# Kernel tuning notes

Hardware: AMD Instinct MI355X
Metric: run time of the kernel (lower is better)

## Reference

```python
import jax, jax.numpy as jnp
import numpy as np

EMB = 1024
HID = 1536
NE = 8


def setup_inputs() -> dict:
    key = jax.random.key(0)
    ks = jax.random.split(key, 8)
    B, N, E, H, ne = 4, 2048, EMB, HID, NE
    s = 1.0 / np.sqrt(E)
    sh = 1.0 / np.sqrt(H)
    return {
        "x": jax.random.normal(ks[0], (B, N, E), dtype=jnp.float32),
        "Wr": jax.random.uniform(ks[1], (E, ne), minval=-s, maxval=s, dtype=jnp.float32),
        "br": jax.random.uniform(ks[2], (ne,), minval=-s, maxval=s, dtype=jnp.float32),
        "W1": jax.random.uniform(ks[3], (ne, E, H), minval=-s, maxval=s, dtype=jnp.float32),
        "b1": jax.random.uniform(ks[4], (ne, H), minval=-s, maxval=s, dtype=jnp.float32),
        "W2": jax.random.uniform(ks[5], (ne, H, E), minval=-sh, maxval=sh, dtype=jnp.float32),
        "b2": jax.random.uniform(ks[6], (ne, E), minval=-sh, maxval=sh, dtype=jnp.float32),
        "k": 2,
    }


def reference(x, Wr, br, W1, b1, W2, b2, k):
    B, N, E = x.shape
    T = B * N
    ne = Wr.shape[1]
    flat = x.reshape(T, E)
    logits = flat @ Wr + br                      # [T, ne]
    _, topk_idx = jax.lax.top_k(logits, k)       # [T, k]
    # counts[t, e] = number of top-k slots of token t assigned to expert e
    counts = jax.nn.one_hot(topk_idx, ne, dtype=flat.dtype).sum(axis=1)  # [T, ne]
    out = jnp.zeros_like(flat)
    for e in range(ne):  # small fixed loop over experts (structurally distinct weights)
        h = jax.nn.gelu(flat @ W1[e] + b1[e], approximate=False)  # torch nn.GELU = exact erf
        y = h @ W2[e] + b2[e]
        out = out + counts[:, e:e + 1] * y
    out = out / k
    return out.reshape(B, N, E)
```

## Files before the change

kernel.cpp:

```cpp
#include <hip/hip_runtime.h>
#include <hip/hip_bf16.h>
#include <math.h>

#define T_TOK 8192
#define EMB   1024
#define HID   1536
#define NE    8
#define NBINB 64
#define BINTOK (T_TOK / NBINB)

typedef float  floatx4 __attribute__((ext_vector_type(4)));
typedef __bf16 bf16x8  __attribute__((ext_vector_type(8)));

#define WS_COUNTS   0
#define WS_OFFSETS  1024
#define WS_FLAGS    2048
#define WS_BHIST    4096
#define WS_TOKMAP   8192
#define WS_TOKLIST  270336
#define WS_YBUF     532480
#define WS_W1T      34086912
#define WS_W2T      59252736
#define WS_H        84418560
#define WS_NEEDED   135143424

__device__ __forceinline__ float eload(const void* p, size_t idx, bool f32) {
  return f32 ? ((const float*)p)[idx] : (float)(((const __bf16*)p)[idx]);
}

__device__ __forceinline__ void glds16(const void* g, void* l) {
  __builtin_amdgcn_global_load_lds(
      (const __attribute__((address_space(1))) unsigned int*)g,
      (__attribute__((address_space(3))) unsigned int*)l, 16, 0, 0);
}

__global__ __launch_bounds__(256)
void sniff_kernel(const void* p0, const void* p1, const void* p2, const void* p3,
                  const void* p4, const void* p5, const void* p6, int* flags) {
  const void* ps[7] = {p0, p1, p2, p3, p4, p5, p6};
  const int nelem[7] = {T_TOK * EMB, EMB * NE, NE, NE * EMB * HID, NE * HID, NE * HID * EMB, NE * EMB};
  int t = blockIdx.x;
  const unsigned* w = (const unsigned*)ps[t];
  int nw = nelem[t] / 2;
  if (nw > 2048) nw = 2048;
  __shared__ int s_pl, s_nz;
  if (threadIdx.x == 0) { s_pl = 0; s_nz = 0; }
  __syncthreads();
  int pl = 0, nz = 0;
  for (int i = threadIdx.x; i < nw; i += 256) {
    unsigned v = w[i];
    if (v == 0) continue;
    nz++;
    unsigned e = (v >> 23) & 0xFF;
    if (e >= 100 && e <= 150) pl++;
  }
  atomicAdd(&s_pl, pl);
  atomicAdd(&s_nz, nz);
  __syncthreads();
  if (threadIdx.x == 0) flags[t] = (2 * s_pl > s_nz) ? 1 : 0;
}

__global__ __launch_bounds__(256)
void logits_kernel(const void* __restrict__ x, const void* __restrict__ Wr,
                   const void* __restrict__ br, const int* __restrict__ kptr,
                   const int* __restrict__ flags, int* __restrict__ topk,
                   __bf16* __restrict__ xbf) {
  const bool xf32  = flags[0] != 0;
  const bool wrf32 = flags[1] != 0;
  const bool brf32 = flags[2] != 0;
  const int wave = threadIdx.x >> 6;
  const int lane = threadIdx.x & 63;
  const int t = blockIdx.x * 4 + wave;

  float xv[16];
  {
    size_t base = (size_t)t * EMB + lane * 16;
    if (xf32) {
      const float* g = (const float*)x + base;
#pragma unroll
      for (int j = 0; j < 16; ++j) xv[j] = g[j];
    } else {
      bf16x8 u = *(const bf16x8*)((const __bf16*)x + base);
      bf16x8 v = *(const bf16x8*)((const __bf16*)x + base + 8);
#pragma unroll
      for (int j = 0; j < 8; ++j) { xv[j] = (float)u[j]; xv[8 + j] = (float)v[j]; }
    }
  }
  {
    bf16x8 o0, o1;
#pragma unroll
    for (int j = 0; j < 8; ++j) { o0[j] = (__bf16)xv[j]; o1[j] = (__bf16)xv[8 + j]; }
    __bf16* xo = xbf + (size_t)t * EMB + lane * 16;
    *(bf16x8*)xo = o0;
    *(bf16x8*)(xo + 8) = o1;
  }
  float acc[NE];
#pragma unroll
  for (int e = 0; e < NE; ++e) acc[e] = 0.f;
  if (wrf32) {
#pragma unroll
    for (int j = 0; j < 16; ++j) {
      const float* wr = (const float*)Wr + (size_t)(lane * 16 + j) * NE;
#pragma unroll
      for (int e = 0; e < NE; ++e) acc[e] += xv[j] * wr[e];
    }
  } else {
#pragma unroll
    for (int j = 0; j < 16; ++j) {
      bf16x8 wr = *(const bf16x8*)((const __bf16*)Wr + (size_t)(lane * 16 + j) * NE);
#pragma unroll
      for (int e = 0; e < NE; ++e) acc[e] += xv[j] * (float)wr[e];
    }
  }
#pragma unroll
  for (int e = 0; e < NE; ++e) {
#pragma unroll
    for (int off = 32; off > 0; off >>= 1)
      acc[e] += __shfl_xor(acc[e], off, 64);
  }
  if (lane == 0) {
    int k = kptr[0];
    if (k < 1) k = 1; if (k > NE) k = NE;
    float lg[NE];
#pragma unroll
    for (int e = 0; e < NE; ++e) lg[e] = acc[e] + eload(br, e, brf32);
    for (int s = 0; s < k; ++s) {
      int bi = 0; float bv = lg[0];
#pragma unroll
      for (int e = 1; e < NE; ++e) { if (lg[e] > bv) { bv = lg[e]; bi = e; } }
      lg[bi] = -3.0e38f;
      topk[t * 8 + s] = bi;
    }
  }
}

__global__ __launch_bounds__(128)
void bin1_kernel(const int* __restrict__ topk, const int* __restrict__ kptr,
                 int* __restrict__ bhist) {
  __shared__ int lhist[NE];
  if (threadIdx.x < NE) lhist[threadIdx.x] = 0;
  __syncthreads();
  int k = kptr[0];
  if (k < 1) k = 1; if (k > NE) k = NE;
  const int t = blockIdx.x * BINTOK + threadIdx.x;
  for (int s = 0; s < k; ++s) atomicAdd(&lhist[topk[t * 8 + s] & 7], 1);
  __syncthreads();
  if (threadIdx.x < NE) bhist[blockIdx.x * NE + threadIdx.x] = lhist[threadIdx.x];
}

__global__ __launch_bounds__(256)
void scan_kernel(int* __restrict__ bhist, int* __restrict__ counts, int* __restrict__ offsets) {
  __shared__ int sh[NBINB * NE];
  __shared__ int scnt[NE];
  __shared__ int soff[NE + 1];
  const int tid = threadIdx.x;
  for (int i = tid; i < NBINB * NE; i += 256) sh[i] = bhist[i];
  __syncthreads();
  if (tid < NE) {
    int s = 0;
    for (int b = 0; b < NBINB; ++b) s += sh[b * NE + tid];
    scnt[tid] = s;
  }
  __syncthreads();
  if (tid == 0) {
    int s = 0;
    for (int e = 0; e < NE; ++e) { soff[e] = s; s += scnt[e]; }
    soff[NE] = s;
  }
  __syncthreads();
  if (tid < NE) {
    int run = soff[tid];
    for (int b = 0; b < NBINB; ++b) {
      int v = sh[b * NE + tid];
      sh[b * NE + tid] = run;
      run += v;
    }
  }
  __syncthreads();
  for (int i = tid; i < NBINB * NE; i += 256) bhist[i] = sh[i];
  if (tid < NE) counts[tid] = scnt[tid];
  if (tid < NE + 1) offsets[tid] = soff[tid];
}

__global__ __launch_bounds__(128)
void bin2_kernel(const int* __restrict__ bhist, const int* __restrict__ offsets,
                 const int* __restrict__ kptr,
                 int* __restrict__ tok_list, int* __restrict__ tokmap) {
  __shared__ int lbase[NE];
  __shared__ int lcnt[NE];
  if (threadIdx.x < NE) {
    lbase[threadIdx.x] = bhist[blockIdx.x * NE + threadIdx.x];
    lcnt[threadIdx.x] = 0;
  }
  __syncthreads();
  int k = kptr[0];
  if (k < 1) k = 1; if (k > NE) k = NE;
  const int t = blockIdx.x * BINTOK + threadIdx.x;
  for (int s = 0; s < k; ++s) {
    int e = tokmap[t * 8 + s] & 7;
    int pos = atomicAdd(&lcnt[e], 1);
    int grow = lbase[e] + pos;
    tok_list[e * T_TOK + (grow - offsets[e])] = t;
    tokmap[t * 8 + s] = (e << 16) | grow;
  }
}

__global__ __launch_bounds__(256)
void transpose_kernel(const void* __restrict__ in, __bf16* __restrict__ out, int K, int N,
                      const int* __restrict__ flags, int fidx) {
  const bool f32 = flags[fidx] != 0;
  __shared__ __bf16 tile[64][65];
  size_t eoff = (size_t)blockIdx.z * (size_t)K * (size_t)N;
  int n0 = blockIdx.x * 64;
  int k0 = blockIdx.y * 64;
  int tx = threadIdx.x & 63;
  int ty = threadIdx.x >> 6;
#pragma unroll
  for (int i = 0; i < 16; ++i) {
    int r = i * 4 + ty;
    tile[r][tx] = (__bf16)eload(in, eoff + (size_t)(k0 + r) * N + (n0 + tx), f32);
  }
  __syncthreads();
#pragma unroll
  for (int i = 0; i < 16; ++i) {
    int r = i * 4 + ty;
    out[eoff + (size_t)(n0 + r) * K + (k0 + tx)] = tile[tx][r];
  }
}


#define STAGE4(TT) do {                                                  \
    const int _sl = (TT) & 3;                                            \
    __bf16* _dA = ldsA + _sl * 8192 + wave * 512;                        \
    __bf16* _dB = ldsB + _sl * 8192 + wave * 512;                        \
    const size_t _ko = (size_t)(TT) * 32;                                \
    glds16(pA0 + _ko, _dA);                                              \
    glds16(pA1 + _ko, _dA + 4096);                                       \
    glds16(pB0 + _ko, _dB);                                              \
    glds16(pB1 + _ko, _dB + 4096);                                       \
  } while (0)

#define KSTEP(TT, WAITS, DOSTAGE) do {                                   \
    asm volatile(WAITS ::: "memory");                                    \
    __builtin_amdgcn_s_barrier();                                        \
    const char* _aS = (const char*)(ldsA + ((TT) & 3) * 8192);           \
    const char* _bS = (const char*)(ldsB + ((TT) & 3) * 8192);           \
    bf16x8 _af[8], _bf[4];                                               \
    _Pragma("unroll")                                                    \
    for (int _i = 0; _i < 8; ++_i) _af[_i] = *(const bf16x8*)(_aS + aOff[_i]); \
    _Pragma("unroll")                                                    \
    for (int _j = 0; _j < 4; ++_j) _bf[_j] = *(const bf16x8*)(_bS + bOff[_j]); \
    if (DOSTAGE) STAGE4((TT) + 3);                                       \
    __builtin_amdgcn_s_setprio(1);                                       \
    _Pragma("unroll")                                                    \
    for (int _i = 0; _i < 8; ++_i)                                       \
      _Pragma("unroll")                                                  \
      for (int _j = 0; _j < 4; ++_j)                                     \
        acc[_i][_j] = __builtin_amdgcn_mfma_f32_16x16x32_bf16(_af[_i], _bf[_j], acc[_i][_j], 0, 0, 0); \
    __builtin_amdgcn_s_setprio(0);                                       \
  } while (0)

__global__ __launch_bounds__(512, 2)
void gemm1_kernel(const __bf16* __restrict__ xbf, const __bf16* __restrict__ w1t,
                  const void* __restrict__ b1, const int* __restrict__ counts,
                  const int* __restrict__ offsets, const int* __restrict__ tok_list,
                  const int* __restrict__ flags, __bf16* __restrict__ hbuf) {
  const int flat = blockIdx.x;
  const int e   = flat & 7;
  const int idx = flat >> 3;
  const int mT  = idx / 6;
  const int nT  = idx % 6;
  const int cnt = counts[e];
  if (mT * 256 >= cnt) return;
  const bool b1f32 = flags[4] != 0;

  __shared__ __align__(16) __bf16 ldsA[4 * 8192];
  __shared__ __align__(16) __bf16 ldsB[4 * 8192];

  const int tid  = threadIdx.x;
  const int wave = tid >> 6;
  const int lane = tid & 63;

  const int sr = wave * 16 + (lane >> 2);
  const int cA = lane & 3;
  const int cg = cA ^ ((sr >> 1) & 3);
  const int tokA0 = tok_list[e * T_TOK + mT * 256 + sr];
  const int tokA1 = tok_list[e * T_TOK + mT * 256 + 128 + sr];
  const __bf16* pA0 = xbf + (size_t)tokA0 * EMB + cg * 8;
  const __bf16* pA1 = xbf + (size_t)tokA1 * EMB + cg * 8;
  const __bf16* pB0 = w1t + ((size_t)e * HID + nT * 256 + sr) * EMB + cg * 8;
  const __bf16* pB1 = w1t + ((size_t)e * HID + nT * 256 + 128 + sr) * EMB + cg * 8;

  const int wm = (wave >> 2) * 128;
  const int wn = (wave & 3) * 64;
  const int fr = lane & 15;
  const int fc = lane >> 4;
  int aOff[8], bOff[4];
#pragma unroll
  for (int i = 0; i < 8; ++i) { int R = wm + i * 16 + fr; aOff[i] = R * 64 + ((fc ^ ((R >> 1) & 3)) << 4); }
#pragma unroll
  for (int j = 0; j < 4; ++j) { int R = wn + j * 16 + fr; bOff[j] = R * 64 + ((fc ^ ((R >> 1) & 3)) << 4); }

  floatx4 acc[8][4];
#pragma unroll
  for (int i = 0; i < 8; ++i)
#pragma unroll
    for (int j = 0; j < 4; ++j) acc[i][j] = (floatx4){0.f, 0.f, 0.f, 0.f};

  STAGE4(0); STAGE4(1); STAGE4(2);
  const int nk = EMB / 32;
#pragma unroll 2
  for (int t = 0; t < nk - 2; ++t) KSTEP(t, "s_waitcnt vmcnt(8)", (t + 3 < nk));
  KSTEP(nk - 2, "s_waitcnt vmcnt(4)", 0);
  KSTEP(nk - 1, "s_waitcnt vmcnt(0)", 0);

  const int hBase   = offsets[e] + mT * 256;
  const int colBase = nT * 256 + wn + fr;
  float bv[4];
#pragma unroll
  for (int j = 0; j < 4; ++j) bv[j] = eload(b1, (size_t)e * HID + colBase + j * 16, b1f32);
#pragma unroll
  for (int i = 0; i < 8; ++i) {
    const int rowLoc = wm + i * 16 + fc * 4;
#pragma unroll
    for (int r = 0; r < 4; ++r) {
      const int row = rowLoc + r;
      if (mT * 256 + row < cnt) {
        __bf16* hp = hbuf + (size_t)(hBase + row) * HID + colBase;
#pragma unroll
        for (int j = 0; j < 4; ++j) {
          float v = acc[i][j][r] + bv[j];
          float g = 0.5f * v * (1.0f + erff(v * 0.70710678118654752f));
          hp[j * 16] = (__bf16)g;
        }
      }
    }
  }
}

__global__ __launch_bounds__(512, 2)
void gemm2_kernel(const __bf16* __restrict__ hbuf, const __bf16* __restrict__ w2t,
                  const void* __restrict__ b2, const int* __restrict__ counts,
                  const int* __restrict__ offsets, const int* __restrict__ flags,
                  __bf16* __restrict__ ybuf) {
  const int flat = blockIdx.x;
  const int e   = flat & 7;
  const int idx = flat >> 3;
  const int mT  = idx >> 2;
  const int nT  = idx & 3;
  const int cnt = counts[e];
  if (mT * 256 >= cnt) return;
  const bool b2f32 = flags[6] != 0;

  __shared__ __align__(16) __bf16 ldsA[4 * 8192];
  __shared__ __align__(16) __bf16 ldsB[4 * 8192];

  const int tid  = threadIdx.x;
  const int wave = tid >> 6;
  const int lane = tid & 63;

  const int sr = wave * 16 + (lane >> 2);
  const int cA = lane & 3;
  const int cg = cA ^ ((sr >> 1) & 3);
  const int rowBase = offsets[e] + mT * 256;
  const int lastRow = offsets[NE] - 1;
  const int rA0 = min(rowBase + sr, lastRow);
  const int rA1 = min(rowBase + 128 + sr, lastRow);
  const __bf16* pA0 = hbuf + (size_t)rA0 * HID + cg * 8;
  const __bf16* pA1 = hbuf + (size_t)rA1 * HID + cg * 8;
  const __bf16* pB0 = w2t + ((size_t)e * EMB + nT * 256 + sr) * HID + cg * 8;
  const __bf16* pB1 = w2t + ((size_t)e * EMB + nT * 256 + 128 + sr) * HID + cg * 8;

  const int wm = (wave >> 2) * 128;
  const int wn = (wave & 3) * 64;
  const int fr = lane & 15;
  const int fc = lane >> 4;
  int aOff[8], bOff[4];
#pragma unroll
  for (int i = 0; i < 8; ++i) { int R = wm + i * 16 + fr; aOff[i] = R * 64 + ((fc ^ ((R >> 1) & 3)) << 4); }
#pragma unroll
  for (int j = 0; j < 4; ++j) { int R = wn + j * 16 + fr; bOff[j] = R * 64 + ((fc ^ ((R >> 1) & 3)) << 4); }

  floatx4 acc[8][4];
#pragma unroll
  for (int i = 0; i < 8; ++i)
#pragma unroll
    for (int j = 0; j < 4; ++j) acc[i][j] = (floatx4){0.f, 0.f, 0.f, 0.f};

  STAGE4(0); STAGE4(1); STAGE4(2);
  const int nk = HID / 32;
#pragma unroll 2
  for (int t = 0; t < nk - 2; ++t) KSTEP(t, "s_waitcnt vmcnt(8)", (t + 3 < nk));
  KSTEP(nk - 2, "s_waitcnt vmcnt(4)", 0);
  KSTEP(nk - 1, "s_waitcnt vmcnt(0)", 0);

  const int colBase = nT * 256 + wn + fr;
  float bv[4];
#pragma unroll
  for (int j = 0; j < 4; ++j) bv[j] = eload(b2, (size_t)e * EMB + colBase + j * 16, b2f32);
#pragma unroll
  for (int i = 0; i < 8; ++i) {
    const int rowLoc = wm + i * 16 + fc * 4;
#pragma unroll
    for (int r = 0; r < 4; ++r) {
      const int row = rowLoc + r;
      if (mT * 256 + row < cnt) {
        __bf16* yp = ybuf + (size_t)(rowBase + row) * EMB + colBase;
#pragma unroll
        for (int j = 0; j < 4; ++j)
          yp[j * 16] = (__bf16)(acc[i][j][r] + bv[j]);
      }
    }
  }
}

__global__ __launch_bounds__(256)
void combine_kernel(const __bf16* __restrict__ ybuf, const int* __restrict__ tokmap,
                    const int* __restrict__ kptr, const int* __restrict__ flags,
                    void* __restrict__ out) {
  const bool f32 = flags[0] != 0;
  const int wave = threadIdx.x >> 6;
  const int lane = threadIdx.x & 63;
  const int t = blockIdx.x * 4 + wave;
  int k = kptr[0];
  if (k < 1) k = 1; if (k > NE) k = NE;
  const float invk = 1.0f / (float)k;
  int rows[NE];
  for (int s = 0; s < k; ++s) rows[s] = tokmap[t * 8 + s] & 0xFFFF;
#pragma unroll
  for (int c = 0; c < 2; ++c) {
    const int i = c * 512 + lane * 8;
    float a[8];
#pragma unroll
    for (int j = 0; j < 8; ++j) a[j] = 0.f;
    for (int s = 0; s < k; ++s) {
      bf16x8 y = *(const bf16x8*)(ybuf + (size_t)rows[s] * EMB + i);
#pragma unroll
      for (int j = 0; j < 8; ++j) a[j] += (float)y[j];
    }
    if (f32) {
      float* op = (float*)out + (size_t)t * EMB + i;
      float4 u = {a[0] * invk, a[1] * invk, a[2] * invk, a[3] * invk};
      float4 v = {a[4] * invk, a[5] * invk, a[6] * invk, a[7] * invk};
      *(float4*)op = u;
      *(float4*)(op + 4) = v;
    } else {
      bf16x8 o;
#pragma unroll
      for (int j = 0; j < 8; ++j) o[j] = (__bf16)(a[j] * invk);
      *(bf16x8*)((__bf16*)out + (size_t)t * EMB + i) = o;
    }
  }
}

extern "C" void kernel_launch(void* const* d_in, const int* in_sizes, int n_in,
                              void* d_out, int out_size, void* d_ws, size_t ws_size,
                              hipStream_t stream) {
  (void)in_sizes; (void)n_in; (void)out_size;
  if (ws_size < (size_t)WS_NEEDED) return;

  const void* x  = d_in[0];
  const void* Wr = d_in[1];
  const void* br = d_in[2];
  const void* W1 = d_in[3];
  const void* b1 = d_in[4];
  const void* W2 = d_in[5];
  const void* b2 = d_in[6];
  const int* kptr = (const int*)d_in[7];

  char* ws = (char*)d_ws;
  int*    counts   = (int*)(ws + WS_COUNTS);
  int*    offsets  = (int*)(ws + WS_OFFSETS);
  int*    flags    = (int*)(ws + WS_FLAGS);
  int*    bhist    = (int*)(ws + WS_BHIST);
  int*    tokmap   = (int*)(ws + WS_TOKMAP);
  int*    tok_list = (int*)(ws + WS_TOKLIST);
  __bf16* ybuf     = (__bf16*)(ws + WS_YBUF);
  __bf16* xbf      = (__bf16*)(ws + WS_YBUF);
  __bf16* w1t      = (__bf16*)(ws + WS_W1T);
  __bf16* w2t      = (__bf16*)(ws + WS_W2T);
  __bf16* hbuf     = (__bf16*)(ws + WS_H);

  hipMemsetAsync(ws, 0, WS_YBUF, stream);

  sniff_kernel<<<dim3(7), 256, 0, stream>>>(x, Wr, br, W1, b1, W2, b2, flags);

  transpose_kernel<<<dim3(HID / 64, EMB / 64, NE), 256, 0, stream>>>(W1, w1t, EMB, HID, flags, 3);
  transpose_kernel<<<dim3(EMB / 64, HID / 64, NE), 256, 0, stream>>>(W2, w2t, HID, EMB, flags, 5);

  logits_kernel<<<dim3(T_TOK / 4), 256, 0, stream>>>(x, Wr, br, kptr, flags, tokmap, xbf);
  bin1_kernel<<<dim3(NBINB), 128, 0, stream>>>(tokmap, kptr, bhist);
  scan_kernel<<<dim3(1), 256, 0, stream>>>(bhist, counts, offsets);
  bin2_kernel<<<dim3(NBINB), 128, 0, stream>>>(bhist, offsets, kptr, tok_list, tokmap);

  gemm1_kernel<<<dim3(8 * 32 * 6), 512, 0, stream>>>(
      xbf, w1t, b1, counts, offsets, tok_list, flags, hbuf);
  gemm2_kernel<<<dim3(8 * 32 * 4), 512, 0, stream>>>(
      hbuf, w2t, b2, counts, offsets, flags, ybuf);

  combine_kernel<<<dim3(T_TOK / 4), 256, 0, stream>>>(ybuf, tokmap, kptr, flags, d_out);
}
```

Baseline: 424.8 us.

## Shrink MoE GEMM M-tile to 128, use 3-stage LDS, persistent M loop

Both expert GEMMs now use 128x256 tiles instead of 256x256, with a three-slot LDS ring (prefetch distance 2) in place of four slots. Launch bounds rise to 4 blocks per CU, and a fixed grid of 16 M-groups per expert/N-tile loops over M tiles in steps of 16. The aim is to cut LDS and register use for higher occupancy and to balance work across uneven expert counts without launching many empty blocks. In exchange, each tile reuses weight data less, and the shallower pipeline may expose more memory latency.

```diff
diff --git a/kernel.cpp b/kernel.cpp
--- a/kernel.cpp
+++ b/kernel.cpp
@@ -229,38 +229,32 @@
 }
 
 
-#define STAGE4(TT) do {                                                  \
-    const int _sl = (TT) & 3;                                            \
-    __bf16* _dA = ldsA + _sl * 8192 + wave * 512;                        \
-    __bf16* _dB = ldsB + _sl * 8192 + wave * 512;                        \
-    const size_t _ko = (size_t)(TT) * 32;                                \
-    glds16(pA0 + _ko, _dA);                                              \
-    glds16(pA1 + _ko, _dA + 4096);                                       \
-    glds16(pB0 + _ko, _dB);                                              \
-    glds16(pB1 + _ko, _dB + 4096);                                       \
+#define STAGE3(SL, KO) do {                                              \
+    __bf16* _d = lds + (SL) * 12288 + wave * 512;                        \
+    glds16(pA0 + (KO), _d);                                              \
+    glds16(pB0 + (KO), _d + 4096);                                       \
+    glds16(pB1 + (KO), _d + 8192);                                       \
   } while (0)
 
-#define KSTEP(TT, WAITS, DOSTAGE) do {                                   \
-    asm volatile(WAITS ::: "memory");                                    \
-    __builtin_amdgcn_s_barrier();                                        \
-    const char* _aS = (const char*)(ldsA + ((TT) & 3) * 8192);           \
-    const char* _bS = (const char*)(ldsB + ((TT) & 3) * 8192);           \
-    bf16x8 _af[8], _bf[4];                                               \
+#define KBODY(SL, DOSTAGE, TT) do {                                      \
+    const char* _s = (const char*)lds + (SL) * 24576;                    \
+    bf16x8 _af[4], _bf[4];                                               \
     _Pragma("unroll")                                                    \
-    for (int _i = 0; _i < 8; ++_i) _af[_i] = *(const bf16x8*)(_aS + aOff[_i]); \
+    for (int _i = 0; _i < 4; ++_i) _af[_i] = *(const bf16x8*)(_s + aOff[_i]); \
     _Pragma("unroll")                                                    \
-    for (int _j = 0; _j < 4; ++_j) _bf[_j] = *(const bf16x8*)(_bS + bOff[_j]); \
-    if (DOSTAGE) STAGE4((TT) + 3);                                       \
+    for (int _j = 0; _j < 4; ++_j) _bf[_j] = *(const bf16x8*)(_s + bOff[_j]); \
+    if (DOSTAGE) { int _sl2 = (SL) == 0 ? 2 : (SL) - 1;                  \
+                   STAGE3(_sl2, (size_t)((TT) + 2) * 32); }              \
     __builtin_amdgcn_s_setprio(1);                                       \
     _Pragma("unroll")                                                    \
-    for (int _i = 0; _i < 8; ++_i)                                       \
+    for (int _i = 0; _i < 4; ++_i)                                       \
       _Pragma("unroll")                                                  \
       for (int _j = 0; _j < 4; ++_j)                                     \
         acc[_i][_j] = __builtin_amdgcn_mfma_f32_16x16x32_bf16(_af[_i], _bf[_j], acc[_i][_j], 0, 0, 0); \
     __builtin_amdgcn_s_setprio(0);                                       \
   } while (0)
 
-__global__ __launch_bounds__(512, 2)
+__global__ __launch_bounds__(512, 4)
 void gemm1_kernel(const __bf16* __restrict__ xbf, const __bf16* __restrict__ w1t,
                   const void* __restrict__ b1, const int* __restrict__ counts,
                   const int* __restrict__ offsets, const int* __restrict__ tok_list,
@@ -268,77 +262,81 @@
   const int flat = blockIdx.x;
   const int e   = flat & 7;
   const int idx = flat >> 3;
-  const int mT  = idx / 6;
+  const int g   = idx / 6;
   const int nT  = idx % 6;
   const int cnt = counts[e];
-  if (mT * 256 >= cnt) return;
   const bool b1f32 = flags[4] != 0;
 
-  __shared__ __align__(16) __bf16 ldsA[4 * 8192];
-  __shared__ __align__(16) __bf16 ldsB[4 * 8192];
-
-  const int tid  = threadIdx.x;
-  const int wave = tid >> 6;
-  const int lane = tid & 63;
-
+  __shared__ __align__(16) __bf16 lds[3 * 12288];
+
+  const int wave = threadIdx.x >> 6;
+  const int lane = threadIdx.x & 63;
   const int sr = wave * 16 + (lane >> 2);
-  const int cA = lane & 3;
-  const int cg = cA ^ ((sr >> 1) & 3);
-  const int tokA0 = tok_list[e * T_TOK + mT * 256 + sr];
-  const int tokA1 = tok_list[e * T_TOK + mT * 256 + 128 + sr];
-  const __bf16* pA0 = xbf + (size_t)tokA0 * EMB + cg * 8;
-  const __bf16* pA1 = xbf + (size_t)tokA1 * EMB + cg * 8;
+  const int cg = (lane & 3) ^ ((sr >> 1) & 3);
+
   const __bf16* pB0 = w1t + ((size_t)e * HID + nT * 256 + sr) * EMB + cg * 8;
   const __bf16* pB1 = w1t + ((size_t)e * HID + nT * 256 + 128 + sr) * EMB + cg * 8;
 
-  const int wm = (wave >> 2) * 128;
+  const int wm = (wave >> 2) * 64;
   const int wn = (wave & 3) * 64;
   const int fr = lane & 15;
   const int fc = lane >> 4;
-  int aOff[8], bOff[4];
-#pragma unroll
-  for (int i = 0; i < 8; ++i) { int R = wm + i * 16 + fr; aOff[i] = R * 64 + ((fc ^ ((R >> 1) & 3)) << 4); }
-#pragma unroll
-  for (int j = 0; j < 4; ++j) { int R = wn + j * 16 + fr; bOff[j] = R * 64 + ((fc ^ ((R >> 1) & 3)) << 4); }
-
-  floatx4 acc[8][4];
-#pragma unroll
-  for (int i = 0; i < 8; ++i)
-#pragma unroll
-    for (int j = 0; j < 4; ++j) acc[i][j] = (floatx4){0.f, 0.f, 0.f, 0.f};
-
-  STAGE4(0); STAGE4(1); STAGE4(2);
-  const int nk = EMB / 32;
-#pragma unroll 2
-  for (int t = 0; t < nk - 2; ++t) KSTEP(t, "s_waitcnt vmcnt(8)", (t + 3 < nk));
-  KSTEP(nk - 2, "s_waitcnt vmcnt(4)", 0);
-  KSTEP(nk - 1, "s_waitcnt vmcnt(0)", 0);
-
-  const int hBase   = offsets[e] + mT * 256;
+  int aOff[4], bOff[4];
+#pragma unroll
+  for (int i = 0; i < 4; ++i) { int R = wm + i * 16 + fr; aOff[i] = R * 64 + ((fc ^ ((R >> 1) & 3)) << 4); }
+#pragma unroll
+  for (int j = 0; j < 4; ++j) { int R = wn + j * 16 + fr; bOff[j] = 8192 + R * 64 + ((fc ^ ((R >> 1) & 3)) << 4); }
+
   const int colBase = nT * 256 + wn + fr;
   float bv[4];
 #pragma unroll
   for (int j = 0; j < 4; ++j) bv[j] = eload(b1, (size_t)e * HID + colBase + j * 16, b1f32);
-#pragma unroll
-  for (int i = 0; i < 8; ++i) {
-    const int rowLoc = wm + i * 16 + fc * 4;
-#pragma unroll
-    for (int r = 0; r < 4; ++r) {
-      const int row = rowLoc + r;
-      if (mT * 256 + row < cnt) {
-        __bf16* hp = hbuf + (size_t)(hBase + row) * HID + colBase;
-#pragma unroll
-        for (int j = 0; j < 4; ++j) {
-          float v = acc[i][j][r] + bv[j];
-          float g = 0.5f * v * (1.0f + erff(v * 0.70710678118654752f));
-          hp[j * 16] = (__bf16)g;
+
+  for (int mT = g; mT * 128 < cnt; mT += 16) {
+    const int tokA = tok_list[e * T_TOK + mT * 128 + sr];
+    const __bf16* pA0 = xbf + (size_t)tokA * EMB + cg * 8;
+
+    floatx4 acc[4][4];
+#pragma unroll
+    for (int i = 0; i < 4; ++i)
+#pragma unroll
+      for (int j = 0; j < 4; ++j) acc[i][j] = (floatx4){0.f, 0.f, 0.f, 0.f};
+
+    __syncthreads();
+    STAGE3(0, 0); STAGE3(1, 32);
+    int sl = 0;
+    for (int t = 0; t < 31; ++t) {
+      asm volatile("s_waitcnt vmcnt(3)" ::: "memory");
+      __builtin_amdgcn_s_barrier();
+      KBODY(sl, (t + 2 < 32), t);
+      sl = (sl + 1 == 3) ? 0 : sl + 1;
+    }
+    asm volatile("s_waitcnt vmcnt(0)" ::: "memory");
+    __builtin_amdgcn_s_barrier();
+    KBODY(sl, 0, 0);
+
+    const int hBase = offsets[e] + mT * 128;
+#pragma unroll
+    for (int i = 0; i < 4; ++i) {
+      const int rowLoc = wm + i * 16 + fc * 4;
+#pragma unroll
+      for (int r = 0; r < 4; ++r) {
+        const int row = rowLoc + r;
+        if (mT * 128 + row < cnt) {
+          __bf16* hp = hbuf + (size_t)(hBase + row) * HID + colBase;
+#pragma unroll
+          for (int j = 0; j < 4; ++j) {
+            float v = acc[i][j][r] + bv[j];
+            float gl = 0.5f * v * (1.0f + erff(v * 0.70710678118654752f));
+            hp[j * 16] = (__bf16)gl;
+          }
         }
       }
     }
   }
 }
 
-__global__ __launch_bounds__(512, 2)
+__global__ __launch_bounds__(512, 4)
 void gemm2_kernel(const __bf16* __restrict__ hbuf, const __bf16* __restrict__ w2t,
                   const void* __restrict__ b2, const int* __restrict__ counts,
                   const int* __restrict__ offsets, const int* __restrict__ flags,
@@ -346,69 +344,74 @@
   const int flat = blockIdx.x;
   const int e   = flat & 7;
   const int idx = flat >> 3;
-  const int mT  = idx >> 2;
+  const int g   = idx >> 2;
   const int nT  = idx & 3;
   const int cnt = counts[e];
-  if (mT * 256 >= cnt) return;
   const bool b2f32 = flags[6] != 0;
 
-  __shared__ __align__(16) __bf16 ldsA[4 * 8192];
-  __shared__ __align__(16) __bf16 ldsB[4 * 8192];
-
-  const int tid  = threadIdx.x;
-  const int wave = tid >> 6;
-  const int lane = tid & 63;
-
+  __shared__ __align__(16) __bf16 lds[3 * 12288];
+
+  const int wave = threadIdx.x >> 6;
+  const int lane = threadIdx.x & 63;
   const int sr = wave * 16 + (lane >> 2);
-  const int cA = lane & 3;
-  const int cg = cA ^ ((sr >> 1) & 3);
-  const int rowBase = offsets[e] + mT * 256;
-  const int lastRow = offsets[NE] - 1;
-  const int rA0 = min(rowBase + sr, lastRow);
-  const int rA1 = min(rowBase + 128 + sr, lastRow);
-  const __bf16* pA0 = hbuf + (size_t)rA0 * HID + cg * 8;
-  const __bf16* pA1 = hbuf + (size_t)rA1 * HID + cg * 8;
+  const int cg = (lane & 3) ^ ((sr >> 1) & 3);
+
   const __bf16* pB0 = w2t + ((size_t)e * EMB + nT * 256 + sr) * HID + cg * 8;
   const __bf16* pB1 = w2t + ((size_t)e * EMB + nT * 256 + 128 + sr) * HID + cg * 8;
 
-  const int wm = (wave >> 2) * 128;
+  const int wm = (wave >> 2) * 64;
   const int wn = (wave & 3) * 64;
   const int fr = lane & 15;
   const int fc = lane >> 4;
-  int aOff[8], bOff[4];
-#pragma unroll
-  for (int i = 0; i < 8; ++i) { int R = wm + i * 16 + fr; aOff[i] = R * 64 + ((fc ^ ((R >> 1) & 3)) << 4); }
-#pragma unroll
-  for (int j = 0; j < 4; ++j) { int R = wn + j * 16 + fr; bOff[j] = R * 64 + ((fc ^ ((R >> 1) & 3)) << 4); }
-
-  floatx4 acc[8][4];
-#pragma unroll
-  for (int i = 0; i < 8; ++i)
-#pragma unroll
-    for (int j = 0; j < 4; ++j) acc[i][j] = (floatx4){0.f, 0.f, 0.f, 0.f};
-
-  STAGE4(0); STAGE4(1); STAGE4(2);
-  const int nk = HID / 32;
-#pragma unroll 2
-  for (int t = 0; t < nk - 2; ++t) KSTEP(t, "s_waitcnt vmcnt(8)", (t + 3 < nk));
-  KSTEP(nk - 2, "s_waitcnt vmcnt(4)", 0);
-  KSTEP(nk - 1, "s_waitcnt vmcnt(0)", 0);
+  int aOff[4], bOff[4];
+#pragma unroll
+  for (int i = 0; i < 4; ++i) { int R = wm + i * 16 + fr; aOff[i] = R * 64 + ((fc ^ ((R >> 1) & 3)) << 4); }
+#pragma unroll
+  for (int j = 0; j < 4; ++j) { int R = wn + j * 16 + fr; bOff[j] = 8192 + R * 64 + ((fc ^ ((R >> 1) & 3)) << 4); }
 
   const int colBase = nT * 256 + wn + fr;
   float bv[4];
 #pragma unroll
   for (int j = 0; j < 4; ++j) bv[j] = eload(b2, (size_t)e * EMB + colBase + j * 16, b2f32);
-#pragma unroll
-  for (int i = 0; i < 8; ++i) {
-    const int rowLoc = wm + i * 16 + fc * 4;
-#pragma unroll
-    for (int r = 0; r < 4; ++r) {
-      const int row = rowLoc + r;
-      if (mT * 256 + row < cnt) {
-        __bf16* yp = ybuf + (size_t)(rowBase + row) * EMB + colBase;
-#pragma unroll
-        for (int j = 0; j < 4; ++j)
-          yp[j * 16] = (__bf16)(acc[i][j][r] + bv[j]);
+
+  const int lastRow = offsets[NE] - 1;
+
+  for (int mT = g; mT * 128 < cnt; mT += 16) {
+    const int rowBase = offsets[e] + mT * 128;
+    const int rA = min(rowBase + sr, lastRow);
+    const __bf16* pA0 = hbuf + (size_t)rA * HID + cg * 8;
+
+    floatx4 acc[4][4];
+#pragma unroll
+    for (int i = 0; i < 4; ++i)
+#pragma unroll
+      for (int j = 0; j < 4; ++j) acc[i][j] = (floatx4){0.f, 0.f, 0.f, 0.f};
+
+    __syncthreads();
+    STAGE3(0, 0); STAGE3(1, 32);
+    int sl = 0;
+    for (int t = 0; t < 47; ++t) {
+      asm volatile("s_waitcnt vmcnt(3)" ::: "memory");
+      __builtin_amdgcn_s_barrier();
+      KBODY(sl, (t + 2 < 48), t);
+      sl = (sl + 1 == 3) ? 0 : sl + 1;
+    }
+    asm volatile("s_waitcnt vmcnt(0)" ::: "memory");
+    __builtin_amdgcn_s_barrier();
+    KBODY(sl, 0, 0);
+
+#pragma unroll
+    for (int i = 0; i < 4; ++i) {
+      const int rowLoc = wm + i * 16 + fc * 4;
+#pragma unroll
+      for (int r = 0; r < 4; ++r) {
+        const int row = rowLoc + r;
+        if (mT * 128 + row < cnt) {
+          __bf16* yp = ybuf + (size_t)(rowBase + row) * EMB + colBase;
+#pragma unroll
+          for (int j = 0; j < 4; ++j)
+            yp[j * 16] = (__bf16)(acc[i][j][r] + bv[j]);
+        }
       }
     }
   }
@@ -493,9 +496,9 @@
   scan_kernel<<<dim3(1), 256, 0, stream>>>(bhist, counts, offsets);
   bin2_kernel<<<dim3(NBINB), 128, 0, stream>>>(bhist, offsets, kptr, tok_list, tokmap);
 
-  gemm1_kernel<<<dim3(8 * 32 * 6), 512, 0, stream>>>(
+  gemm1_kernel<<<dim3(8 * 16 * 6), 512, 0, stream>>>(
       xbf, w1t, b1, counts, offsets, tok_list, flags, hbuf);
-  gemm2_kernel<<<dim3(8 * 32 * 4), 512, 0, stream>>>(
+  gemm2_kernel<<<dim3(8 * 16 * 4), 512, 0, stream>>>(
       hbuf, w2t, b2, counts, offsets, flags, ybuf);
 
   combine_kernel<<<dim3(T_TOK / 4), 256, 0, stream>>>(ybuf, tokmap, kptr, flags, d_out);
```

New measurement: 441.0 us. 1.04x slower.
